# Kernel tuning notes

Hardware: AMD Instinct MI355X
Metric: run time of the kernel (lower is better)

The kernel has to match this reference:

```python
import jax, jax.numpy as jnp
import numpy as np

T, B, IN, H, L = 512, 32, 512, 512, 2  # seq_len, batch, input_size, hidden_size, num_layers
D = 2  # bidirectional
EPS = 1e-5


def setup_inputs() -> dict:
    key = jax.random.key(0)
    ks = jax.random.split(key, 4)
    s = 0.05
    return {
        "x": jax.random.normal(ks[0], (T, B, IN), jnp.float32),
        "h0": jnp.zeros((L * D, B, H), jnp.float32),
        # stacked per (layer, direction) params; index = 2*layer + dir (dir 0 = fwd, 1 = back)
        "Wx": jax.random.normal(ks[1], (L * D, IN, 3 * H), jnp.float32) * s,
        "Wh": jax.random.normal(ks[2], (L * D, H, 3 * H), jnp.float32) * s,
        "bx": jnp.zeros((L * D, 3 * H), jnp.float32),
        "bh": jnp.zeros((L * D, 3 * H), jnp.float32),
        "gx": jnp.ones((L * D, 3 * H), jnp.float32),   # LN affine scale for input proj
        "bex": jnp.zeros((L * D, 3 * H), jnp.float32), # LN affine shift for input proj
        "gh": jnp.ones((L * D, 3 * H), jnp.float32),   # LN affine scale for recurrent proj
        "beh": jnp.zeros((L * D, 3 * H), jnp.float32), # LN affine shift for recurrent proj
    }


def _ln3(a, g, b):
    # per-gate LayerNorm: a is [B, 3H]; normalize each H-sized gate chunk
    Bn, H3 = a.shape
    Hh = H3 // 3
    a = a.reshape(Bn, 3, Hh)
    mu = a.mean(-1, keepdims=True)
    var = ((a - mu) ** 2).mean(-1, keepdims=True)
    a = (a - mu) * jax.lax.rsqrt(var + EPS)
    a = a * g.reshape(3, Hh) + b.reshape(3, Hh)
    return a.reshape(Bn, H3)


def _run_dir(xs, h, Wx, Wh, bx, bh, gx, bex, gh, beh):
    # xs: [T, B, F], h: [B, H]; scan LNGRU cell over time
    def step(h, x):
        ax = _ln3(x @ Wx + bx, gx, bex)
        ah = _ln3(h @ Wh + bh, gh, beh)
        axr, axz, axn = jnp.split(ax, 3, axis=-1)
        ahr, ahz, ahn = jnp.split(ah, 3, axis=-1)
        r = jax.nn.sigmoid(axr + ahr)
        z = jax.nn.sigmoid(axz + ahz)
        n = jnp.tanh(axn + r * ahn)
        h_new = (1.0 - z) * n + z * h
        return h_new, h_new
    hT, ys = jax.lax.scan(step, h, xs)
    return hT, ys


def reference(x, h0, Wx, Wh, bx, bh, gx, bex, gh, beh):
    ff, back = x, x
    hiddens = []
    for layer in range(L):
        i = 2 * layer
        hT, ff = _run_dir(ff, h0[i], Wx[i], Wh[i], bx[i], bh[i], gx[i], bex[i], gh[i], beh[i])
        hiddens.append(hT)
        j = 2 * layer + 1
        hT, yb = _run_dir(back[::-1], h0[j], Wx[j], Wh[j], bx[j], bh[j], gx[j], bex[j], gh[j], beh[j])
        back = yb[::-1]
        hiddens.append(hT)
    output = jnp.concatenate([ff, back], axis=-1)  # [T, B, 2H]
    return output, jnp.stack(hiddens)  # hiddens: [L*2, B, H]
```

## Files before the change

kernel.cpp:

```cpp
#include <hip/hip_runtime.h>

#define T_N 512
#define B_N 32
#define H_N 512
#define G3 1536
#define NBLK 192
#define NGRP 8
#define GRPSZ (NBLK / NGRP)
#define NT 1024
#define EPS_LN 1e-5f
#define OUT_HID_OFF (T_N * B_N * 1024)

#define WS_STATS 832
#define STSLOT   768
#define WS_AXD   (WS_STATS + 4 * STSLOT)
#define DSLOT    (2 * B_N * G3)
#define WS_AHD   (WS_AXD + 2 * DSLOT)
#define WS_HBUF  (WS_AHD + 2 * DSLOT)
#define WS_Y0    (WS_HBUF + 2 * B_N * H_N)

#define WLDS_F 32256
#define HL_F   8256
#define LDS_BYTES ((WLDS_F + HL_F + 256) * 4)

__device__ __forceinline__ float cload(const float* p) {
  return __hip_atomic_load(p, __ATOMIC_RELAXED, __HIP_MEMORY_SCOPE_AGENT);
}
__device__ __forceinline__ void cstore(float* p, float v) {
  __hip_atomic_store(p, v, __ATOMIC_RELAXED, __HIP_MEMORY_SCOPE_AGENT);
}
union U64F2 { unsigned long long u; float f[2]; };
__device__ __forceinline__ U64F2 cload2(const float* p) {
  U64F2 r;
  r.u = __hip_atomic_load((const unsigned long long*)p, __ATOMIC_RELAXED,
                          __HIP_MEMORY_SCOPE_AGENT);
  return r;
}

__device__ __forceinline__ void gbar(unsigned* barbase, unsigned& epoch, int grp) {
  epoch++;
  __builtin_amdgcn_s_waitcnt(0);
  __syncthreads();
  if (threadIdx.x == 0) {
    unsigned* gc  = barbase + grp * 32;
    unsigned* top = barbase + 256;
    unsigned* rel = barbase + 288;
    unsigned r = __hip_atomic_fetch_add(gc, 1u, __ATOMIC_RELAXED, __HIP_MEMORY_SCOPE_AGENT);
    if (r == epoch * GRPSZ - 1u) {
      unsigned r2 = __hip_atomic_fetch_add(top, 1u, __ATOMIC_RELAXED, __HIP_MEMORY_SCOPE_AGENT);
      if (r2 == epoch * NGRP - 1u)
        __hip_atomic_store(rel, epoch, __ATOMIC_RELAXED, __HIP_MEMORY_SCOPE_AGENT);
    }
    while (__hip_atomic_load(rel, __ATOMIC_RELAXED, __HIP_MEMORY_SCOPE_AGENT) < epoch)
      __builtin_amdgcn_s_sleep(1);
  }
  __syncthreads();
}

__device__ __forceinline__ void gbar2_arrive(unsigned* b2, unsigned& e2, int grp) {
  e2++;
  __builtin_amdgcn_s_waitcnt(0);
  __syncthreads();
  if (threadIdx.x == 0) {
    unsigned r = __hip_atomic_fetch_add(b2 + grp * 32, 1u, __ATOMIC_RELAXED, __HIP_MEMORY_SCOPE_AGENT);
    if (r == e2 * 4u - 1u) {
      unsigned r2 = __hip_atomic_fetch_add(b2 + 256, 1u, __ATOMIC_RELAXED, __HIP_MEMORY_SCOPE_AGENT);
      if (r2 == e2 * 8u - 1u)
        __hip_atomic_store(b2 + 288, e2, __ATOMIC_RELAXED, __HIP_MEMORY_SCOPE_AGENT);
    }
  }
}

__device__ __forceinline__ void gbar2_wait(unsigned* b2, unsigned& e2) {
  e2++;
  if (threadIdx.x == 0) {
    while (__hip_atomic_load(b2 + 288, __ATOMIC_RELAXED, __HIP_MEMORY_SCOPE_AGENT) < e2)
      __builtin_amdgcn_s_sleep(1);
  }
  __syncthreads();
}

#define FMA_M(M, W, R1, R2) do { \
  acc[M][0][0]=fmaf((R1).x,(W).x,acc[M][0][0]); acc[M][0][1]=fmaf((R1).y,(W).y,acc[M][0][1]); \
  acc[M][0][2]=fmaf((R1).z,(W).z,acc[M][0][2]); acc[M][0][3]=fmaf((R1).w,(W).w,acc[M][0][3]); \
  acc[M][1][0]=fmaf((R2).x,(W).x,acc[M][1][0]); acc[M][1][1]=fmaf((R2).y,(W).y,acc[M][1][1]); \
  acc[M][1][2]=fmaf((R2).z,(W).z,acc[M][1][2]); acc[M][1][3]=fmaf((R2).w,(W).w,acc[M][1][3]); \
} while (0)

__global__ void __launch_bounds__(NT, 1)
lngru11(const float* __restrict__ x, const float* __restrict__ h0,
        const float* __restrict__ Wx, const float* __restrict__ Wh,
        const float* __restrict__ bx, const float* __restrict__ bh,
        const float* __restrict__ gx, const float* __restrict__ bex,
        const float* __restrict__ gh, const float* __restrict__ beh,
        float* __restrict__ out, float* __restrict__ ws)
{
  extern __shared__ __align__(16) float smem[];
  float* wlds = smem;
  float* hl   = smem + WLDS_F;
  float* sred = smem + WLDS_F + HL_F;

  unsigned* barbase  = (unsigned*)ws;
  unsigned* barbase2 = barbase + 320;
  float* stats = ws + WS_STATS;
  float* axd   = ws + WS_AXD;
  float* ahd   = ws + WS_AHD;
  float* hbuf  = ws + WS_HBUF;
  float* y0    = ws + WS_Y0;

  const int tid  = threadIdx.x;
  const int lane = tid & 63;
  const int wv   = tid >> 6;
  const int bid  = blockIdx.x;
  const int grp  = bid & 7;
  const int bs   = bid & 1;
  const int jt   = (bid >> 1) % 24;
  const int kd   = (bid >> 1) / 24;
  const int kind = kd & 1;
  const int d    = kd >> 1;
  const int j0   = jt * 64;
  const int g    = jt >> 3;
  const int b0   = bs * 16;
  const bool is_gate = (kind == 0) && (jt < 8);

  const bool gw  = (wv < 2);
  const int jq   = wv & 1;
  const int jj   = lane & 7;
  const int boct = lane >> 3;

  unsigned epoch = 0, epoch2 = 0;

  for (int ph = 0; ph < 2; ++ph) {
    const int widx = ph * 2 + d;

    gbar(barbase, epoch, grp);

    const float* wgl = (kind ? Wh : Wx) + (size_t)widx * H_N * G3 + j0;
    for (int kk = 0; kk < 32; ++kk) {
      int k = wv * 32 + kk;
      if (k < 504)
        wlds[(k >> 2) * 256 + lane * 4 + (k & 3)] = wgl[(size_t)k * G3 + lane];
    }
    float4 wt[4][2];
    float  bva[4];
    if (gw) {
#pragma unroll
      for (int m = 0; m < 4; ++m) {
        const int jl = jq * 32 + m * 8 + jj;
        bva[m] = (kind ? bh : bx)[widx * G3 + j0 + jl];
#pragma unroll
        for (int h = 0; h < 2; ++h) {
          wt[m][h].x = wgl[(size_t)(504 + 4*h + 0) * G3 + jl];
          wt[m][h].y = wgl[(size_t)(504 + 4*h + 1) * G3 + jl];
          wt[m][h].z = wgl[(size_t)(504 + 4*h + 2) * G3 + jl];
          wt[m][h].w = wgl[(size_t)(504 + 4*h + 3) * G3 + jl];
        }
      }
    }
    if (kind) {
#pragma unroll
      for (int q = 0; q < 8; ++q)
        hl[wv * 516 + lane + 64*q] =
            h0[((size_t)widx * B_N + b0 + wv) * H_N + lane + 64*q];
    }
    if (is_gate) {
      cstore(&hbuf[(d * B_N + b0 + wv) * H_N + j0 + lane],
             h0[((size_t)widx * B_N + b0 + wv) * H_N + j0 + lane]);
    }
    __syncthreads();

    const float* xsrc = (ph == 0) ? x : (y0 + (size_t)d * T_N * B_N * H_N);
    const float4* wbase = (const float4*)wlds + jq * 32 + jj;

    auto run_step = [&](int ss) {
      float acc[4][2][4] = {};
      if (gw) {
        if (kind) {
          const float* h1 = hl + boct * 516;
          const float* h2 = h1 + 8 * 516;
#pragma unroll 3
          for (int k4 = 0; k4 < 126; ++k4) {
            float4 w0 = wbase[k4*64 + 0];
            float4 w1 = wbase[k4*64 + 8];
            float4 w2 = wbase[k4*64 + 16];
            float4 w3 = wbase[k4*64 + 24];
            float4 r1 = *(const float4*)(h1 + k4*4);
            float4 r2 = *(const float4*)(h2 + k4*4);
            FMA_M(0,w0,r1,r2); FMA_M(1,w1,r1,r2);
            FMA_M(2,w2,r1,r2); FMA_M(3,w3,r1,r2);
          }
          float4 r1a = *(const float4*)(h1 + 504);
          float4 r1b = *(const float4*)(h1 + 508);
          float4 r2a = *(const float4*)(h2 + 504);
          float4 r2b = *(const float4*)(h2 + 508);
          FMA_M(0,wt[0][0],r1a,r2a); FMA_M(1,wt[1][0],r1a,r2a);
          FMA_M(2,wt[2][0],r1a,r2a); FMA_M(3,wt[3][0],r1a,r2a);
          FMA_M(0,wt[0][1],r1b,r2b); FMA_M(1,wt[1][1],r1b,r2b);
          FMA_M(2,wt[2][1],r1b,r2b); FMA_M(3,wt[3][1],r1b,r2b);
        } else {
          const int t = d ? (T_N - 1 - ss) : ss;
          const float* rp1 = xsrc + ((size_t)t * B_N + b0 + boct) * H_N;
          const float* rp2 = rp1 + 8 * H_N;
#pragma unroll 4
          for (int k4 = 0; k4 < 126; ++k4) {
            float4 w0 = wbase[k4*64 + 0];
            float4 w1 = wbase[k4*64 + 8];
            float4 w2 = wbase[k4*64 + 16];
            float4 w3 = wbase[k4*64 + 24];
            float4 r1 = *(const float4*)(rp1 + k4*4);
            float4 r2 = *(const float4*)(rp2 + k4*4);
            FMA_M(0,w0,r1,r2); FMA_M(1,w1,r1,r2);
            FMA_M(2,w2,r1,r2); FMA_M(3,w3,r1,r2);
          }
          float4 r1a = *(const float4*)(rp1 + 504);
          float4 r1b = *(const float4*)(rp1 + 508);
          float4 r2a = *(const float4*)(rp2 + 504);
          float4 r2b = *(const float4*)(rp2 + 508);
          FMA_M(0,wt[0][0],r1a,r2a); FMA_M(1,wt[1][0],r1a,r2a);
          FMA_M(2,wt[2][0],r1a,r2a); FMA_M(3,wt[3][0],r1a,r2a);
          FMA_M(0,wt[0][1],r1b,r2b); FMA_M(1,wt[1][1],r1b,r2b);
          FMA_M(2,wt[2][1],r1b,r2b); FMA_M(3,wt[3][1],r1b,r2b);
        }
      }
      float* dd  = (kind ? ahd : axd) + (ss & 1) * DSLOT;
      float* stp = stats + (ss & 3) * STSLOT;
      if (gw) {
        float* dr1 = dd + (size_t)(d * B_N + b0 + boct) * G3 + j0;
        float* dr2 = dr1 + (size_t)8 * G3;
        float s1a = 0.f, s2a = 0.f, s1b = 0.f, s2b = 0.f;
#pragma unroll
        for (int m = 0; m < 4; ++m) {
          const int jl = jq * 32 + m * 8 + jj;
          float t1 = bva[m] + ((acc[m][0][0]+acc[m][0][1]) + (acc[m][0][2]+acc[m][0][3]));
          float t2 = bva[m] + ((acc[m][1][0]+acc[m][1][1]) + (acc[m][1][2]+acc[m][1][3]));
          cstore(dr1 + jl, t1);
          cstore(dr2 + jl, t2);
          s1a += t1; s2a += t1 * t1; s1b += t2; s2b += t2 * t2;
        }
        s1a += __shfl_xor(s1a, 1, 64); s2a += __shfl_xor(s2a, 1, 64);
        s1b += __shfl_xor(s1b, 1, 64); s2b += __shfl_xor(s2b, 1, 64);
        s1a += __shfl_xor(s1a, 2, 64); s2a += __shfl_xor(s2a, 2, 64);
        s1b += __shfl_xor(s1b, 2, 64); s2b += __shfl_xor(s2b, 2, 64);
        s1a += __shfl_xor(s1a, 4, 64); s2a += __shfl_xor(s2a, 4, 64);
        s1b += __shfl_xor(s1b, 4, 64); s2b += __shfl_xor(s2b, 4, 64);
        if (jj == 0) {
          sred[boct * 4 + jq * 2 + 0] = s1a;
          sred[boct * 4 + jq * 2 + 1] = s2a;
          sred[(boct + 8) * 4 + jq * 2 + 0] = s1b;
          sred[(boct + 8) * 4 + jq * 2 + 1] = s2b;
        }
      }
      __syncthreads();
      if (tid < 32) {
        int bl = tid >> 1, st = tid & 1;
        float a2 = sred[bl * 4 + st] + sred[bl * 4 + 2 + st];
        atomicAdd(&stp[((kd * 3 + g) * B_N + b0 + bl) * 2 + st], a2);
      }
    };

    run_step(0);

    for (int s = 0; s < T_N; ++s) {
      gbar(barbase, epoch, grp);

      if (bid == NBLK - 1) {
        float* so = stats + ((s + 2) & 3) * STSLOT;
        if (tid < 768) cstore(so + tid, 0.f);
      }

      if (is_gate) {
        const int t  = d ? (T_N - 1 - s) : s;
        const int c  = j0 + lane;
        const int gb = b0 + wv;
        const float* stp = stats + (s & 3) * STSLOT;
        float a[2][3];
#pragma unroll
        for (int k2 = 0; k2 < 2; ++k2) {
          const float* dr  = (k2 ? ahd : axd) + (s & 1) * DSLOT
                             + (size_t)(d * B_N + gb) * G3;
          const float* gam = (k2 ? gh : gx) + widx * G3;
          const float* bet = (k2 ? beh : bex) + widx * G3;
#pragma unroll
          for (int g2 = 0; g2 < 3; ++g2) {
            float v = cload(dr + g2 * H_N + c);
            const float* sl = stp + (((d * 2 + k2) * 3 + g2) * B_N + gb) * 2;
            float mu  = cload(sl)     * (1.f / 512.f);
            float var = cload(sl + 1) * (1.f / 512.f) - mu * mu;
            float inv = rsqrtf(var + EPS_LN);
            int J = g2 * H_N + c;
            a[k2][g2] = (v - mu) * inv * gam[J] + bet[J];
          }
        }
        float r = 1.f / (1.f + __expf(-(a[0][0] + a[1][0])));
        float z = 1.f / (1.f + __expf(-(a[0][1] + a[1][1])));
        float n = tanhf(a[0][2] + r * a[1][2]);
        float* hp = hbuf + (d * B_N + gb) * H_N + c;
        float hnew = (1.f - z) * n + z * cload(hp);
        cstore(hp, hnew);
        if (ph == 0) {
          cstore(&y0[(((size_t)d * T_N + t) * B_N + gb) * H_N + c], hnew);
        } else {
          out[((size_t)t * B_N + gb) * 1024 + d * H_N + c] = hnew;
        }
        if (s == T_N - 1) {
          out[OUT_HID_OFF + ((size_t)widx * B_N + gb) * H_N + c] = hnew;
        }
        gbar2_arrive(barbase2, epoch2, grp);
        if (s < T_N - 1) run_step(s + 1);
      } else if (!kind) {
        if (s < T_N - 1) run_step(s + 1);
      } else {
        gbar2_wait(barbase2, epoch2);
        if (s < T_N - 1) {
          const float* hsrc = hbuf + (d * B_N + b0) * H_N;
#pragma unroll
          for (int q = 0; q < 4; ++q) {
            int e = (tid + q * 1024) * 2;
            U64F2 v = cload2(hsrc + e);
            int bb = e >> 9, k = e & 511;
            hl[bb * 516 + k]     = v.f[0];
            hl[bb * 516 + k + 1] = v.f[1];
          }
          __syncthreads();
          run_step(s + 1);
        }
      }
    }
  }
}

extern "C" void kernel_launch(void* const* d_in, const int* in_sizes, int n_in,
                              void* d_out, int out_size, void* d_ws, size_t ws_size,
                              hipStream_t stream) {
  const float* x    = (const float*)d_in[0];
  const float* h0   = (const float*)d_in[1];
  const float* Wx   = (const float*)d_in[2];
  const float* Wh   = (const float*)d_in[3];
  const float* bxp  = (const float*)d_in[4];
  const float* bhp  = (const float*)d_in[5];
  const float* gxp  = (const float*)d_in[6];
  const float* bexp = (const float*)d_in[7];
  const float* ghp  = (const float*)d_in[8];
  const float* behp = (const float*)d_in[9];
  float* out = (float*)d_out;
  float* ws  = (float*)d_ws;

  hipMemsetAsync(d_ws, 0, 16384, stream);

  hipFuncSetAttribute((const void*)lngru11,
                      hipFuncAttributeMaxDynamicSharedMemorySize, LDS_BYTES);

  void* args[] = {(void*)&x, (void*)&h0, (void*)&Wx, (void*)&Wh, (void*)&bxp, (void*)&bhp,
                  (void*)&gxp, (void*)&bexp, (void*)&ghp, (void*)&behp, (void*)&out, (void*)&ws};
  hipLaunchCooperativeKernel((void*)lngru11, dim3(NBLK), dim3(NT), args, LDS_BYTES, stream);
}
```

Before: 25.30 ms.

## Replace pipelined split-barrier schedule with two full grid barriers per step

Removes the software pipelining in which input-projection blocks computed step s+1 while the gate blocks finished step s, along with the second arrive/wait barrier used for that. Each step now runs the dot products, passes a grid barrier, applies the gates, then passes a second grid barrier. The barrier tree widens from 8 to 16 groups, and the double- and quad-buffered dot and stats slots collapse to single and double buffers. The schedule is simpler and needs less workspace, but the Wx projection no longer overlaps the recurrent critical path, and every block now waits at two full barriers per step.

Result: slower. 36.30 ms (+43.5%).

```diff
diff --git a/kernel.cpp b/kernel.cpp
--- a/kernel.cpp
+++ b/kernel.cpp
@@ -5,18 +5,15 @@
 #define H_N 512
 #define G3 1536
 #define NBLK 192
-#define NGRP 8
+#define NGRP 16
 #define GRPSZ (NBLK / NGRP)
 #define NT 1024
 #define EPS_LN 1e-5f
 #define OUT_HID_OFF (T_N * B_N * 1024)
 
-#define WS_STATS 832
-#define STSLOT   768
-#define WS_AXD   (WS_STATS + 4 * STSLOT)
-#define DSLOT    (2 * B_N * G3)
-#define WS_AHD   (WS_AXD + 2 * DSLOT)
-#define WS_HBUF  (WS_AHD + 2 * DSLOT)
+#define WS_STATS 640
+#define WS_DOTS  (WS_STATS + 1536)
+#define WS_HBUF  (WS_DOTS + 4 * B_N * G3)
 #define WS_Y0    (WS_HBUF + 2 * B_N * H_N)
 
 #define WLDS_F 32256
@@ -43,8 +40,8 @@
   __syncthreads();
   if (threadIdx.x == 0) {
     unsigned* gc  = barbase + grp * 32;
-    unsigned* top = barbase + 256;
-    unsigned* rel = barbase + 288;
+    unsigned* top = barbase + 512;
+    unsigned* rel = barbase + 544;
     unsigned r = __hip_atomic_fetch_add(gc, 1u, __ATOMIC_RELAXED, __HIP_MEMORY_SCOPE_AGENT);
     if (r == epoch * GRPSZ - 1u) {
       unsigned r2 = __hip_atomic_fetch_add(top, 1u, __ATOMIC_RELAXED, __HIP_MEMORY_SCOPE_AGENT);
@@ -52,29 +49,6 @@
         __hip_atomic_store(rel, epoch, __ATOMIC_RELAXED, __HIP_MEMORY_SCOPE_AGENT);
     }
     while (__hip_atomic_load(rel, __ATOMIC_RELAXED, __HIP_MEMORY_SCOPE_AGENT) < epoch)
-      __builtin_amdgcn_s_sleep(1);
-  }
-  __syncthreads();
-}
-
-__device__ __forceinline__ void gbar2_arrive(unsigned* b2, unsigned& e2, int grp) {
-  e2++;
-  __builtin_amdgcn_s_waitcnt(0);
-  __syncthreads();
-  if (threadIdx.x == 0) {
-    unsigned r = __hip_atomic_fetch_add(b2 + grp * 32, 1u, __ATOMIC_RELAXED, __HIP_MEMORY_SCOPE_AGENT);
-    if (r == e2 * 4u - 1u) {
-      unsigned r2 = __hip_atomic_fetch_add(b2 + 256, 1u, __ATOMIC_RELAXED, __HIP_MEMORY_SCOPE_AGENT);
-      if (r2 == e2 * 8u - 1u)
-        __hip_atomic_store(b2 + 288, e2, __ATOMIC_RELAXED, __HIP_MEMORY_SCOPE_AGENT);
-    }
-  }
-}
-
-__device__ __forceinline__ void gbar2_wait(unsigned* b2, unsigned& e2) {
-  e2++;
-  if (threadIdx.x == 0) {
-    while (__hip_atomic_load(b2 + 288, __ATOMIC_RELAXED, __HIP_MEMORY_SCOPE_AGENT) < e2)
       __builtin_amdgcn_s_sleep(1);
   }
   __syncthreads();
@@ -88,7 +62,7 @@
 } while (0)
 
 __global__ void __launch_bounds__(NT, 1)
-lngru11(const float* __restrict__ x, const float* __restrict__ h0,
+lngru12(const float* __restrict__ x, const float* __restrict__ h0,
         const float* __restrict__ Wx, const float* __restrict__ Wh,
         const float* __restrict__ bx, const float* __restrict__ bh,
         const float* __restrict__ gx, const float* __restrict__ bex,
@@ -100,11 +74,9 @@
   float* hl   = smem + WLDS_F;
   float* sred = smem + WLDS_F + HL_F;
 
-  unsigned* barbase  = (unsigned*)ws;
-  unsigned* barbase2 = barbase + 320;
+  unsigned* barbase = (unsigned*)ws;
   float* stats = ws + WS_STATS;
-  float* axd   = ws + WS_AXD;
-  float* ahd   = ws + WS_AHD;
+  float* dots  = ws + WS_DOTS;
   float* hbuf  = ws + WS_HBUF;
   float* y0    = ws + WS_Y0;
 
@@ -112,7 +84,7 @@
   const int lane = tid & 63;
   const int wv   = tid >> 6;
   const int bid  = blockIdx.x;
-  const int grp  = bid & 7;
+  const int grp  = bid & 15;
   const int bs   = bid & 1;
   const int jt   = (bid >> 1) % 24;
   const int kd   = (bid >> 1) / 24;
@@ -128,12 +100,10 @@
   const int jj   = lane & 7;
   const int boct = lane >> 3;
 
-  unsigned epoch = 0, epoch2 = 0;
+  unsigned epoch = 0;
 
   for (int ph = 0; ph < 2; ++ph) {
     const int widx = ph * 2 + d;
-
-    gbar(barbase, epoch, grp);
 
     const float* wgl = (kind ? Wh : Wx) + (size_t)widx * H_N * G3 + j0;
     for (int kk = 0; kk < 32; ++kk) {
@@ -157,22 +127,34 @@
         }
       }
     }
-    if (kind) {
-#pragma unroll
-      for (int q = 0; q < 8; ++q)
-        hl[wv * 516 + lane + 64*q] =
-            h0[((size_t)widx * B_N + b0 + wv) * H_N + lane + 64*q];
-    }
+
     if (is_gate) {
       cstore(&hbuf[(d * B_N + b0 + wv) * H_N + j0 + lane],
              h0[((size_t)widx * B_N + b0 + wv) * H_N + j0 + lane]);
     }
-    __syncthreads();
+    gbar(barbase, epoch, grp);
 
     const float* xsrc = (ph == 0) ? x : (y0 + (size_t)d * T_N * B_N * H_N);
+    const float* hsrc = hbuf + (d * B_N + b0) * H_N;
     const float4* wbase = (const float4*)wlds + jq * 32 + jj;
 
-    auto run_step = [&](int ss) {
+    for (int s = 0; s < T_N; ++s) {
+      const int t = d ? (T_N - 1 - s) : s;
+      const int p = s & 1;
+      float* stp = stats + p * 768;
+
+      if (kind) {
+#pragma unroll
+        for (int q = 0; q < 4; ++q) {
+          int e = (tid + q * 1024) * 2;
+          U64F2 v = cload2(hsrc + e);
+          int bb = e >> 9, k = e & 511;
+          hl[bb * 516 + k]     = v.f[0];
+          hl[bb * 516 + k + 1] = v.f[1];
+        }
+        __syncthreads();
+      }
+
       float acc[4][2][4] = {};
       if (gw) {
         if (kind) {
@@ -198,7 +180,6 @@
           FMA_M(0,wt[0][1],r1b,r2b); FMA_M(1,wt[1][1],r1b,r2b);
           FMA_M(2,wt[2][1],r1b,r2b); FMA_M(3,wt[3][1],r1b,r2b);
         } else {
-          const int t = d ? (T_N - 1 - ss) : ss;
           const float* rp1 = xsrc + ((size_t)t * B_N + b0 + boct) * H_N;
           const float* rp2 = rp1 + 8 * H_N;
 #pragma unroll 4
@@ -221,11 +202,8 @@
           FMA_M(0,wt[0][1],r1b,r2b); FMA_M(1,wt[1][1],r1b,r2b);
           FMA_M(2,wt[2][1],r1b,r2b); FMA_M(3,wt[3][1],r1b,r2b);
         }
-      }
-      float* dd  = (kind ? ahd : axd) + (ss & 1) * DSLOT;
-      float* stp = stats + (ss & 3) * STSLOT;
-      if (gw) {
-        float* dr1 = dd + (size_t)(d * B_N + b0 + boct) * G3 + j0;
+
+        float* dr1 = &dots[(size_t)(kd * B_N + b0 + boct) * G3 + j0];
         float* dr2 = dr1 + (size_t)8 * G3;
         float s1a = 0.f, s2a = 0.f, s1b = 0.f, s2b = 0.f;
 #pragma unroll
@@ -256,28 +234,20 @@
         float a2 = sred[bl * 4 + st] + sred[bl * 4 + 2 + st];
         atomicAdd(&stp[((kd * 3 + g) * B_N + b0 + bl) * 2 + st], a2);
       }
-    };
-
-    run_step(0);
-
-    for (int s = 0; s < T_N; ++s) {
+
       gbar(barbase, epoch, grp);
 
       if (bid == NBLK - 1) {
-        float* so = stats + ((s + 2) & 3) * STSLOT;
+        float* so = stats + (p ^ 1) * 768;
         if (tid < 768) cstore(so + tid, 0.f);
       }
-
       if (is_gate) {
-        const int t  = d ? (T_N - 1 - s) : s;
         const int c  = j0 + lane;
         const int gb = b0 + wv;
-        const float* stp = stats + (s & 3) * STSLOT;
         float a[2][3];
 #pragma unroll
         for (int k2 = 0; k2 < 2; ++k2) {
-          const float* dr  = (k2 ? ahd : axd) + (s & 1) * DSLOT
-                             + (size_t)(d * B_N + gb) * G3;
+          const float* dr  = dots + ((d * 2 + k2) * B_N + gb) * G3;
           const float* gam = (k2 ? gh : gx) + widx * G3;
           const float* bet = (k2 ? beh : bex) + widx * G3;
 #pragma unroll
@@ -305,26 +275,8 @@
         if (s == T_N - 1) {
           out[OUT_HID_OFF + ((size_t)widx * B_N + gb) * H_N + c] = hnew;
         }
-        gbar2_arrive(barbase2, epoch2, grp);
-        if (s < T_N - 1) run_step(s + 1);
-      } else if (!kind) {
-        if (s < T_N - 1) run_step(s + 1);
-      } else {
-        gbar2_wait(barbase2, epoch2);
-        if (s < T_N - 1) {
-          const float* hsrc = hbuf + (d * B_N + b0) * H_N;
-#pragma unroll
-          for (int q = 0; q < 4; ++q) {
-            int e = (tid + q * 1024) * 2;
-            U64F2 v = cload2(hsrc + e);
-            int bb = e >> 9, k = e & 511;
-            hl[bb * 516 + k]     = v.f[0];
-            hl[bb * 516 + k + 1] = v.f[1];
-          }
-          __syncthreads();
-          run_step(s + 1);
-        }
-      }
+      }
+      gbar(barbase, epoch, grp);
     }
   }
 }
@@ -345,12 +297,12 @@
   float* out = (float*)d_out;
   float* ws  = (float*)d_ws;
 
-  hipMemsetAsync(d_ws, 0, 16384, stream);
-
-  hipFuncSetAttribute((const void*)lngru11,
+  hipMemsetAsync(d_ws, 0, 12288, stream);
+
+  hipFuncSetAttribute((const void*)lngru12,
                       hipFuncAttributeMaxDynamicSharedMemorySize, LDS_BYTES);
 
   void* args[] = {(void*)&x, (void*)&h0, (void*)&Wx, (void*)&Wh, (void*)&bxp, (void*)&bhp,
                   (void*)&gxp, (void*)&bexp, (void*)&ghp, (void*)&behp, (void*)&out, (void*)&ws};
-  hipLaunchCooperativeKernel((void*)lngru11, dim3(NBLK), dim3(NT), args, LDS_BYTES, stream);
-}
+  hipLaunchCooperativeKernel((void*)lngru12, dim3(NBLK), dim3(NT), args, LDS_BYTES, stream);
+}
```
